# Optimization experiments

Measured on AMD Instinct MI355X. Metric: run time of the kernel, lower is better.

## Reference

```python
import jax, jax.numpy as jnp
import numpy as np

H = 4096      # hidden_size (also vocab size of the embedding, per source)
O = 4096      # output_size (also embedding dim, per source)
MAX_LEN = 15


def setup_inputs() -> dict:
    key = jax.random.key(0)
    ks = jax.random.split(key, 16)
    s = 0.02  # init scale
    inp = {
        "input_ids": jax.random.randint(ks[0], (1,), 0, H),
        "hidden": jax.random.normal(ks[1], (1, 1, H), jnp.float32),
        "e_output": jax.random.normal(ks[2], (1, H), jnp.float32),   # unused, kept for signature fidelity
        "e_output_seq": jax.random.normal(ks[3], (MAX_LEN, H), jnp.float32),
        # parameters
        "emb_W": jax.random.normal(ks[4], (H, O), jnp.float32) * s,
        "att_W": jax.random.normal(ks[5], (MAX_LEN, H + O), jnp.float32) * s,
        "att_b": jnp.zeros((MAX_LEN,), jnp.float32),
        "comb_W": jax.random.normal(ks[6], (H, H + O), jnp.float32) * s,
        "comb_b": jnp.zeros((H,), jnp.float32),
        "gru_W_ih": jax.random.normal(ks[7], (3 * H, H), jnp.float32) * s,
        "gru_W_hh": jax.random.normal(ks[8], (3 * H, H), jnp.float32) * s,
        "gru_b_ih": jnp.zeros((3 * H,), jnp.float32),
        "gru_b_hh": jnp.zeros((3 * H,), jnp.float32),
        "out_W": jax.random.normal(ks[9], (O, H), jnp.float32) * s,
        "out_b": jnp.zeros((O,), jnp.float32),
    }
    return inp


def reference(input_ids, hidden, e_output, e_output_seq, emb_W, att_W, att_b,
              comb_W, comb_b, gru_W_ih, gru_W_hh, gru_b_ih, gru_b_hh, out_W, out_b):
    # dropout is identity in eval mode
    emb = emb_W[input_ids[0]][None, :]                       # [1, O]
    h0 = hidden[0]                                            # [1, H]
    att_logits = jnp.concatenate([emb, h0], axis=1) @ att_W.T + att_b
    att_weights = jax.nn.softmax(att_logits, axis=-1)         # [1, MAX_LEN]
    att_applied = att_weights @ e_output_seq                   # [1, H]
    combined = jnp.concatenate([emb, att_applied], axis=1)     # [1, H+O]
    x = jax.nn.relu(combined @ comb_W.T + comb_b)              # [1, H]
    # GRU cell (PyTorch gate order: r, z, n)
    gi = x @ gru_W_ih.T + gru_b_ih                             # [1, 3H]
    gh = h0 @ gru_W_hh.T + gru_b_hh                            # [1, 3H]
    i_r, i_z, i_n = jnp.split(gi, 3, axis=1)
    h_r, h_z, h_n = jnp.split(gh, 3, axis=1)
    r = jax.nn.sigmoid(i_r + h_r)
    z = jax.nn.sigmoid(i_z + h_z)
    n = jnp.tanh(i_n + r * h_n)
    h_new = (1.0 - z) * n + z * h0                             # [1, H]
    out = jax.nn.log_softmax(h_new @ out_W.T + out_b, axis=-1)  # [1, O]
    return out, h_new[None, :, :], att_weights
```

## Files before the change

### kernel.cpp

```cpp
#include <hip/hip_runtime.h>

#define H 4096
#define O 4096
#define HO 8192
#define MAXLEN 15

__device__ __forceinline__ float wave_dot(const float* __restrict__ w,
                                          const float* __restrict__ x,
                                          int K, int lane) {
    const float4* w4 = (const float4*)w;
    const float4* x4 = (const float4*)x;
    float acc = 0.f;
    int n4 = K >> 2;
    for (int i = lane; i < n4; i += 64) {
        float4 wv = w4[i];
        float4 xv = x4[i];
        acc += wv.x * xv.x + wv.y * xv.y + wv.z * xv.z + wv.w * xv.w;
    }
    #pragma unroll
    for (int off = 32; off; off >>= 1) acc += __shfl_down(acc, off, 64);
    return acc;
}

__global__ void k_att(const int* __restrict__ ids,
                      const float* __restrict__ hidden,
                      const float* __restrict__ eseq,
                      const float* __restrict__ embW,
                      const float* __restrict__ attW,
                      const float* __restrict__ attb,
                      float* __restrict__ combined,
                      float* __restrict__ out_attw) {
    __shared__ float s_logit[MAXLEN];
    __shared__ float s_w[MAXLEN];
    const int tid  = threadIdx.x;
    const int wave = tid >> 6, lane = tid & 63;
    const int id = ids[0];
    const float* emb = embW + (size_t)id * O;

    for (int k = tid; k < O; k += blockDim.x) combined[k] = emb[k];

    if (wave < MAXLEN) {
        const float* wrow = attW + (size_t)wave * (H + O);
        float acc = 0.f;
        for (int t = lane; t < O; t += 64) acc += emb[t] * wrow[t];
        for (int t = lane; t < H; t += 64) acc += hidden[t] * wrow[O + t];
        #pragma unroll
        for (int off = 32; off; off >>= 1) acc += __shfl_down(acc, off, 64);
        if (lane == 0) s_logit[wave] = acc + attb[wave];
    }
    __syncthreads();
    if (tid == 0) {
        float m = -1e30f;
        for (int j = 0; j < MAXLEN; j++) m = fmaxf(m, s_logit[j]);
        float s = 0.f;
        for (int j = 0; j < MAXLEN; j++) { float e = __expf(s_logit[j] - m); s_w[j] = e; s += e; }
        float inv = 1.f / s;
        for (int j = 0; j < MAXLEN; j++) { s_w[j] *= inv; out_attw[j] = s_w[j]; }
    }
    __syncthreads();
    for (int k = tid; k < H; k += blockDim.x) {
        float acc = 0.f;
        #pragma unroll
        for (int j = 0; j < MAXLEN; j++) acc += s_w[j] * eseq[j * H + k];
        combined[O + k] = acc;
    }
}

__global__ void k_comb_ghh(const float* __restrict__ combW,
                           const float* __restrict__ combB,
                           const float* __restrict__ ghhW,
                           const float* __restrict__ ghhB,
                           const float* __restrict__ hidden,
                           const float* __restrict__ combined,
                           float* __restrict__ xout,
                           float* __restrict__ ghout) {
    const int wave = threadIdx.x >> 6, lane = threadIdx.x & 63;
    const int b = blockIdx.x;
    if (b < 1024) {
        int row = b * 4 + wave;
        float d = wave_dot(combW + (size_t)row * HO, combined, HO, lane);
        if (lane == 0) xout[row] = fmaxf(d + combB[row], 0.f);
    } else {
        int row = (b - 1024) * 4 + wave;
        float d = wave_dot(ghhW + (size_t)row * H, hidden, H, lane);
        if (lane == 0) ghout[row] = d + ghhB[row];
    }
}

__global__ void k_gru(const float* __restrict__ gihW,
                      const float* __restrict__ gihB,
                      const float* __restrict__ hidden,
                      const float* __restrict__ x,
                      const float* __restrict__ gh,
                      float* __restrict__ hout,
                      float* __restrict__ out_h) {
    const int wave = threadIdx.x >> 6, lane = threadIdx.x & 63;
    const int i = blockIdx.x * 4 + wave;
    float d0 = wave_dot(gihW + (size_t)i * H,           x, H, lane);
    float d1 = wave_dot(gihW + (size_t)(i + H) * H,     x, H, lane);
    float d2 = wave_dot(gihW + (size_t)(i + 2 * H) * H, x, H, lane);
    if (lane == 0) {
        float ir = d0 + gihB[i];
        float iz = d1 + gihB[i + H];
        float in_ = d2 + gihB[i + 2 * H];
        float hr = gh[i], hz = gh[i + H], hn = gh[i + 2 * H];
        float r = 1.f / (1.f + __expf(-(ir + hr)));
        float z = 1.f / (1.f + __expf(-(iz + hz)));
        float n = tanhf(in_ + r * hn);
        float h0 = hidden[i];
        float h = (1.f - z) * n + z * h0;
        hout[i] = h;
        out_h[i] = h;
    }
}

__global__ void k_out(const float* __restrict__ outW,
                      const float* __restrict__ outB,
                      const float* __restrict__ h,
                      float* __restrict__ logits) {
    const int wave = threadIdx.x >> 6, lane = threadIdx.x & 63;
    const int i = blockIdx.x * 4 + wave;
    float d = wave_dot(outW + (size_t)i * H, h, H, lane);
    if (lane == 0) logits[i] = d + outB[i];
}

__global__ void k_lsm(const float* __restrict__ logits, float* __restrict__ out) {
    __shared__ float red[16];
    __shared__ float red2[16];
    const int tid = threadIdx.x, lane = tid & 63, wave = tid >> 6;
    float m = -1e30f;
    for (int k = tid; k < O; k += 1024) m = fmaxf(m, logits[k]);
    #pragma unroll
    for (int off = 32; off; off >>= 1) m = fmaxf(m, __shfl_down(m, off, 64));
    if (lane == 0) red[wave] = m;
    __syncthreads();
    if (tid == 0) {
        float mm = -1e30f;
        for (int j = 0; j < 16; j++) mm = fmaxf(mm, red[j]);
        red[0] = mm;
    }
    __syncthreads();
    m = red[0];
    float s = 0.f;
    for (int k = tid; k < O; k += 1024) s += __expf(logits[k] - m);
    #pragma unroll
    for (int off = 32; off; off >>= 1) s += __shfl_down(s, off, 64);
    if (lane == 0) red2[wave] = s;
    __syncthreads();
    if (tid == 0) {
        float ss = 0.f;
        for (int j = 0; j < 16; j++) ss += red2[j];
        red2[0] = m + logf(ss);
    }
    __syncthreads();
    float lse = red2[0];
    for (int k = tid; k < O; k += 1024) out[k] = logits[k] - lse;
}

extern "C" void kernel_launch(void* const* d_in, const int* in_sizes, int n_in,
                              void* d_out, int out_size, void* d_ws, size_t ws_size,
                              hipStream_t stream) {
    const int*   ids    = (const int*)d_in[0];
    const float* hidden = (const float*)d_in[1];
    const float* eseq   = (const float*)d_in[3];
    const float* embW   = (const float*)d_in[4];
    const float* attW   = (const float*)d_in[5];
    const float* attb   = (const float*)d_in[6];
    const float* combW  = (const float*)d_in[7];
    const float* combB  = (const float*)d_in[8];
    const float* gihW   = (const float*)d_in[9];
    const float* ghhW   = (const float*)d_in[10];
    const float* gihB   = (const float*)d_in[11];
    const float* ghhB   = (const float*)d_in[12];
    const float* outW   = (const float*)d_in[13];
    const float* outB   = (const float*)d_in[14];
    float* out = (float*)d_out;

    float* ws       = (float*)d_ws;
    float* combined = ws;
    float* xbuf     = ws + 8192;
    float* ghbuf    = ws + 12288;
    float* hbuf     = ws + 24576;
    float* logits   = ws + 28672;

    k_att     <<<1,    960,  0, stream>>>(ids, hidden, eseq, embW, attW, attb, combined, out + 8192);
    k_comb_ghh<<<4096, 256,  0, stream>>>(combW, combB, ghhW, ghhB, hidden, combined, xbuf, ghbuf);
    k_gru     <<<1024, 256,  0, stream>>>(gihW, gihB, hidden, xbuf, ghbuf, hbuf, out + 4096);
    k_out     <<<1024, 256,  0, stream>>>(outW, outB, hbuf, logits);
    k_lsm     <<<1,    1024, 0, stream>>>(logits, out);
}
```

Before: 614.4 us.

## Split attention into parallel logit/apply kernels and process two rows per wave

```diff
diff --git a/kernel.cpp b/kernel.cpp
--- a/kernel.cpp
+++ b/kernel.cpp
@@ -5,104 +5,151 @@
 #define HO 8192
 #define MAXLEN 15
 
-__device__ __forceinline__ float wave_dot(const float* __restrict__ w,
+__device__ __forceinline__ void wave_dot2(const float* __restrict__ w0,
+                                          const float* __restrict__ w1,
                                           const float* __restrict__ x,
-                                          int K, int lane) {
-    const float4* w4 = (const float4*)w;
-    const float4* x4 = (const float4*)x;
+                                          int n4, int lane,
+                                          float& r0, float& r1) {
+    const float4* a  = (const float4*)w0;
+    const float4* b  = (const float4*)w1;
+    const float4* xx = (const float4*)x;
+    float acc0 = 0.f, acc1 = 0.f;
+    #pragma unroll 4
+    for (int i = lane; i < n4; i += 64) {
+        float4 xv = xx[i];
+        float4 av = a[i];
+        float4 bv = b[i];
+        acc0 += av.x * xv.x + av.y * xv.y + av.z * xv.z + av.w * xv.w;
+        acc1 += bv.x * xv.x + bv.y * xv.y + bv.z * xv.z + bv.w * xv.w;
+    }
+    #pragma unroll
+    for (int off = 32; off; off >>= 1) {
+        acc0 += __shfl_down(acc0, off, 64);
+        acc1 += __shfl_down(acc1, off, 64);
+    }
+    r0 = acc0; r1 = acc1;
+}
+
+__global__ __launch_bounds__(1024) void k_attlogit(const int* __restrict__ ids,
+                                                   const float* __restrict__ hidden,
+                                                   const float* __restrict__ embW,
+                                                   const float* __restrict__ attW,
+                                                   const float* __restrict__ attb,
+                                                   float* __restrict__ attlog) {
+    __shared__ float sred[16];
+    const int tid = threadIdx.x, lane = tid & 63, wave = tid >> 6;
+    const int j = blockIdx.x;
+    const float* emb = embW + (size_t)ids[0] * O;
+    const float4* w4 = (const float4*)(attW + (size_t)j * (H + O));
+    const float4* e4 = (const float4*)emb;
+    const float4* h4 = (const float4*)hidden;
+
+    float4 wv0 = w4[tid];
+    float4 xv0 = e4[tid];
+    float4 wv1 = w4[tid + 1024];
+    float4 xv1 = h4[tid];
+    float acc = wv0.x * xv0.x + wv0.y * xv0.y + wv0.z * xv0.z + wv0.w * xv0.w
+              + wv1.x * xv1.x + wv1.y * xv1.y + wv1.z * xv1.z + wv1.w * xv1.w;
+    #pragma unroll
+    for (int off = 32; off; off >>= 1) acc += __shfl_down(acc, off, 64);
+    if (lane == 0) sred[wave] = acc;
+    __syncthreads();
+    if (tid == 0) {
+        float s = 0.f;
+        #pragma unroll
+        for (int w = 0; w < 16; w++) s += sred[w];
+        attlog[j] = s + attb[j];
+    }
+}
+
+__global__ __launch_bounds__(256) void k_attapply(const int* __restrict__ ids,
+                                                  const float* __restrict__ embW,
+                                                  const float* __restrict__ attlog,
+                                                  const float* __restrict__ eseq,
+                                                  float* __restrict__ combined,
+                                                  float* __restrict__ out_attw) {
+    const int k = blockIdx.x * 256 + threadIdx.x;
+    float l[MAXLEN];
+    float m = -1e30f;
+    #pragma unroll
+    for (int j = 0; j < MAXLEN; j++) { l[j] = attlog[j]; m = fmaxf(m, l[j]); }
+    float s = 0.f;
+    #pragma unroll
+    for (int j = 0; j < MAXLEN; j++) { l[j] = __expf(l[j] - m); s += l[j]; }
+    const float inv = 1.f / s;
+
     float acc = 0.f;
-    int n4 = K >> 2;
-    for (int i = lane; i < n4; i += 64) {
-        float4 wv = w4[i];
-        float4 xv = x4[i];
-        acc += wv.x * xv.x + wv.y * xv.y + wv.z * xv.z + wv.w * xv.w;
-    }
-    #pragma unroll
-    for (int off = 32; off; off >>= 1) acc += __shfl_down(acc, off, 64);
-    return acc;
-}
-
-__global__ void k_att(const int* __restrict__ ids,
-                      const float* __restrict__ hidden,
-                      const float* __restrict__ eseq,
-                      const float* __restrict__ embW,
-                      const float* __restrict__ attW,
-                      const float* __restrict__ attb,
-                      float* __restrict__ combined,
-                      float* __restrict__ out_attw) {
-    __shared__ float s_logit[MAXLEN];
-    __shared__ float s_w[MAXLEN];
-    const int tid  = threadIdx.x;
-    const int wave = tid >> 6, lane = tid & 63;
-    const int id = ids[0];
-    const float* emb = embW + (size_t)id * O;
-
-    for (int k = tid; k < O; k += blockDim.x) combined[k] = emb[k];
-
-    if (wave < MAXLEN) {
-        const float* wrow = attW + (size_t)wave * (H + O);
-        float acc = 0.f;
-        for (int t = lane; t < O; t += 64) acc += emb[t] * wrow[t];
-        for (int t = lane; t < H; t += 64) acc += hidden[t] * wrow[O + t];
-        #pragma unroll
-        for (int off = 32; off; off >>= 1) acc += __shfl_down(acc, off, 64);
-        if (lane == 0) s_logit[wave] = acc + attb[wave];
-    }
-    __syncthreads();
-    if (tid == 0) {
-        float m = -1e30f;
-        for (int j = 0; j < MAXLEN; j++) m = fmaxf(m, s_logit[j]);
-        float s = 0.f;
-        for (int j = 0; j < MAXLEN; j++) { float e = __expf(s_logit[j] - m); s_w[j] = e; s += e; }
-        float inv = 1.f / s;
-        for (int j = 0; j < MAXLEN; j++) { s_w[j] *= inv; out_attw[j] = s_w[j]; }
-    }
-    __syncthreads();
-    for (int k = tid; k < H; k += blockDim.x) {
-        float acc = 0.f;
-        #pragma unroll
-        for (int j = 0; j < MAXLEN; j++) acc += s_w[j] * eseq[j * H + k];
-        combined[O + k] = acc;
-    }
-}
-
-__global__ void k_comb_ghh(const float* __restrict__ combW,
-                           const float* __restrict__ combB,
-                           const float* __restrict__ ghhW,
-                           const float* __restrict__ ghhB,
-                           const float* __restrict__ hidden,
-                           const float* __restrict__ combined,
-                           float* __restrict__ xout,
-                           float* __restrict__ ghout) {
+    #pragma unroll
+    for (int j = 0; j < MAXLEN; j++) acc += l[j] * eseq[j * H + k];
+    combined[O + k] = acc * inv;
+    combined[k] = embW[(size_t)ids[0] * O + k];
+    if (blockIdx.x == 0 && threadIdx.x < MAXLEN) out_attw[threadIdx.x] = l[threadIdx.x] * inv;
+}
+
+__global__ __launch_bounds__(512) void k_mv1(const float* __restrict__ combW,
+                                             const float* __restrict__ combB,
+                                             const float* __restrict__ ghhW,
+                                             const float* __restrict__ ghhB,
+                                             const float* __restrict__ hidden,
+                                             const float* __restrict__ combined,
+                                             float* __restrict__ xout,
+                                             float* __restrict__ ghout) {
     const int wave = threadIdx.x >> 6, lane = threadIdx.x & 63;
     const int b = blockIdx.x;
-    if (b < 1024) {
-        int row = b * 4 + wave;
-        float d = wave_dot(combW + (size_t)row * HO, combined, HO, lane);
-        if (lane == 0) xout[row] = fmaxf(d + combB[row], 0.f);
+    float r0, r1;
+    if (b < 256) {
+        const int row = b * 16 + wave * 2;
+        wave_dot2(combW + (size_t)row * HO, combW + (size_t)(row + 1) * HO,
+                  combined, HO >> 2, lane, r0, r1);
+        if (lane == 0) {
+            xout[row]     = fmaxf(r0 + combB[row], 0.f);
+            xout[row + 1] = fmaxf(r1 + combB[row + 1], 0.f);
+        }
     } else {
-        int row = (b - 1024) * 4 + wave;
-        float d = wave_dot(ghhW + (size_t)row * H, hidden, H, lane);
-        if (lane == 0) ghout[row] = d + ghhB[row];
-    }
-}
-
-__global__ void k_gru(const float* __restrict__ gihW,
-                      const float* __restrict__ gihB,
-                      const float* __restrict__ hidden,
-                      const float* __restrict__ x,
-                      const float* __restrict__ gh,
-                      float* __restrict__ hout,
-                      float* __restrict__ out_h) {
+        const int row = (b - 256) * 16 + wave * 2;
+        wave_dot2(ghhW + (size_t)row * H, ghhW + (size_t)(row + 1) * H,
+                  hidden, H >> 2, lane, r0, r1);
+        if (lane == 0) {
+            ghout[row]     = r0 + ghhB[row];
+            ghout[row + 1] = r1 + ghhB[row + 1];
+        }
+    }
+}
+
+__global__ __launch_bounds__(256) void k_gru(const float* __restrict__ gihW,
+                                             const float* __restrict__ gihB,
+                                             const float* __restrict__ hidden,
+                                             const float* __restrict__ x,
+                                             const float* __restrict__ gh,
+                                             float* __restrict__ hout,
+                                             float* __restrict__ out_h) {
     const int wave = threadIdx.x >> 6, lane = threadIdx.x & 63;
     const int i = blockIdx.x * 4 + wave;
-    float d0 = wave_dot(gihW + (size_t)i * H,           x, H, lane);
-    float d1 = wave_dot(gihW + (size_t)(i + H) * H,     x, H, lane);
-    float d2 = wave_dot(gihW + (size_t)(i + 2 * H) * H, x, H, lane);
+    const float4* w0 = (const float4*)(gihW + (size_t)i * H);
+    const float4* w1 = (const float4*)(gihW + (size_t)(i + H) * H);
+    const float4* w2 = (const float4*)(gihW + (size_t)(i + 2 * H) * H);
+    const float4* x4 = (const float4*)x;
+    float a0 = 0.f, a1 = 0.f, a2 = 0.f;
+    #pragma unroll 4
+    for (int t = lane; t < (H >> 2); t += 64) {
+        float4 xv = x4[t];
+        float4 v0 = w0[t];
+        float4 v1 = w1[t];
+        float4 v2 = w2[t];
+        a0 += v0.x * xv.x + v0.y * xv.y + v0.z * xv.z + v0.w * xv.w;
+        a1 += v1.x * xv.x + v1.y * xv.y + v1.z * xv.z + v1.w * xv.w;
+        a2 += v2.x * xv.x + v2.y * xv.y + v2.z * xv.z + v2.w * xv.w;
+    }
+    #pragma unroll
+    for (int off = 32; off; off >>= 1) {
+        a0 += __shfl_down(a0, off, 64);
+        a1 += __shfl_down(a1, off, 64);
+        a2 += __shfl_down(a2, off, 64);
+    }
     if (lane == 0) {
-        float ir = d0 + gihB[i];
-        float iz = d1 + gihB[i + H];
-        float in_ = d2 + gihB[i + 2 * H];
+        float ir = a0 + gihB[i];
+        float iz = a1 + gihB[i + H];
+        float in_ = a2 + gihB[i + 2 * H];
         float hr = gh[i], hz = gh[i + H], hn = gh[i + 2 * H];
         float r = 1.f / (1.f + __expf(-(ir + hr)));
         float z = 1.f / (1.f + __expf(-(iz + hz)));
@@ -114,17 +161,22 @@
     }
 }
 
-__global__ void k_out(const float* __restrict__ outW,
-                      const float* __restrict__ outB,
-                      const float* __restrict__ h,
-                      float* __restrict__ logits) {
+__global__ __launch_bounds__(512) void k_out(const float* __restrict__ outW,
+                                             const float* __restrict__ outB,
+                                             const float* __restrict__ h,
+                                             float* __restrict__ logits) {
     const int wave = threadIdx.x >> 6, lane = threadIdx.x & 63;
-    const int i = blockIdx.x * 4 + wave;
-    float d = wave_dot(outW + (size_t)i * H, h, H, lane);
-    if (lane == 0) logits[i] = d + outB[i];
-}
-
-__global__ void k_lsm(const float* __restrict__ logits, float* __restrict__ out) {
+    const int row = blockIdx.x * 16 + wave * 2;
+    float r0, r1;
+    wave_dot2(outW + (size_t)row * H, outW + (size_t)(row + 1) * H, h, H >> 2, lane, r0, r1);
+    if (lane == 0) {
+        logits[row]     = r0 + outB[row];
+        logits[row + 1] = r1 + outB[row + 1];
+    }
+}
+
+__global__ __launch_bounds__(1024) void k_lsm(const float* __restrict__ logits,
+                                              float* __restrict__ out) {
     __shared__ float red[16];
     __shared__ float red2[16];
     const int tid = threadIdx.x, lane = tid & 63, wave = tid >> 6;
@@ -182,10 +234,12 @@
     float* ghbuf    = ws + 12288;
     float* hbuf     = ws + 24576;
     float* logits   = ws + 28672;
-
-    k_att     <<<1,    960,  0, stream>>>(ids, hidden, eseq, embW, attW, attb, combined, out + 8192);
-    k_comb_ghh<<<4096, 256,  0, stream>>>(combW, combB, ghhW, ghhB, hidden, combined, xbuf, ghbuf);
-    k_gru     <<<1024, 256,  0, stream>>>(gihW, gihB, hidden, xbuf, ghbuf, hbuf, out + 4096);
-    k_out     <<<1024, 256,  0, stream>>>(outW, outB, hbuf, logits);
-    k_lsm     <<<1,    1024, 0, stream>>>(logits, out);
-}
+    float* attlog   = ws + 32768;
+
+    k_attlogit<<<MAXLEN, 1024, 0, stream>>>(ids, hidden, embW, attW, attb, attlog);
+    k_attapply<<<16,     256,  0, stream>>>(ids, embW, attlog, eseq, combined, out + 8192);
+    k_mv1     <<<1024,   512,  0, stream>>>(combW, combB, ghhW, ghhB, hidden, combined, xbuf, ghbuf);
+    k_gru     <<<1024,   256,  0, stream>>>(gihW, gihB, hidden, xbuf, ghbuf, hbuf, out + 4096);
+    k_out     <<<256,    512,  0, stream>>>(outW, outB, hbuf, logits);
+    k_lsm     <<<1,      1024, 0, stream>>>(logits, out);
+}
```

Result: faster. 566.0 us (-7.9%).
